# Optimization experiments

Measured on AMD Instinct MI355X. Metric: run time of the kernel, lower is better.

## Reference

```python
import jax, jax.numpy as jnp
import numpy as np

B, S, D = 128, 512, 512  # source requires S == hidden_dim for bmm(Q^T, K^T) to type-check


def setup_inputs() -> dict:
    key = jax.random.key(0)
    ks = jax.random.split(key, 7)
    scale = 1.0 / np.sqrt(D)
    return {
        "x": jax.random.normal(ks[0], (B, S, D), dtype=jnp.float32),
        "Wq": jax.random.uniform(ks[1], (D, D), jnp.float32, -scale, scale),
        "bq": jax.random.uniform(ks[2], (D,), jnp.float32, -scale, scale),
        "Wk": jax.random.uniform(ks[3], (D, D), jnp.float32, -scale, scale),
        "bk": jax.random.uniform(ks[4], (D,), jnp.float32, -scale, scale),
        "Wv": jax.random.uniform(ks[5], (D, D), jnp.float32, -scale, scale),
        "bv": jax.random.uniform(ks[6], (D,), jnp.float32, -scale, scale),
    }


def reference(x, Wq, bq, Wk, bk, Wv, bv):
    # nn.Linear: y = x @ W^T + b
    Q = jnp.einsum("bsd,ed->bse", x, Wq) + bq  # (B,S,D)
    K = jnp.einsum("bsd,ed->bse", x, Wk) + bk
    V = jnp.einsum("bsd,ed->bse", x, Wv) + bv
    Qp = jnp.transpose(Q, (0, 2, 1))  # (B,D,S)
    Kp = jnp.transpose(K, (0, 2, 1))  # (B,D,S); bmm needs S == D
    energy = jnp.matmul(Qp, Kp)       # (B,D,D) -- unscaled, as in source
    attention = jax.nn.softmax(energy, axis=2)
    Vp = jnp.transpose(V, (0, 2, 1))  # (B,D,S)
    context = jnp.matmul(attention, Vp)  # (B,D,S)
    return jnp.transpose(context, (0, 2, 1))  # (B,S,D)
```

## Files before the change

kernel.cpp:

```cpp
#include <hip/hip_runtime.h>
#include <hip/hip_bf16.h>


#define NDIM 512
#define NBATCH 128
constexpr size_t SD = (size_t)NDIM * NDIM;

typedef __attribute__((ext_vector_type(8))) short bf16x8;
typedef __attribute__((ext_vector_type(4))) float f32x4;

typedef const __attribute__((address_space(1))) unsigned int* gas_ptr;
typedef __attribute__((address_space(3))) unsigned int* las_ptr;

struct alignas(8) us4 { unsigned short x, y, z, w; };

__device__ __forceinline__ void gl_lds16(const void* g, void* lds) {
    __builtin_amdgcn_global_load_lds((gas_ptr)g, (las_ptr)lds, 16, 0, 0);
}
__device__ __forceinline__ unsigned short f2bf(float x) {
    return __builtin_bit_cast(unsigned short, __float2bfloat16(x));
}
__device__ __forceinline__ float bf2f(unsigned short u) {
    return __bfloat162float(__builtin_bit_cast(__hip_bfloat16, u));
}

template<int EPI, int BIAS>
__global__ __launch_bounds__(512, 2) void gemm8_fused3(
    const unsigned short* aH, const unsigned short* aL, long sA,
    const unsigned short* bH, const unsigned short* bL, long sB,
    void* c0v, void* c1v, long sC, const float* __restrict__ bias)
{
    constexpr int NTK = 16;
    __shared__ unsigned short AHs[2][8192];
    __shared__ unsigned short ALs[2][8192];
    __shared__ unsigned short BHs[2][8192];
    __shared__ unsigned short BLs[2][8192];

    const int nwg = gridDim.x;
    int id = blockIdx.x;
    int wg = ((nwg & 7) == 0) ? ((id & 7) * (nwg >> 3) + (id >> 3)) : id;
    const int z  = wg >> 2;
    const int m0 = ((wg >> 1) & 1) * 256;
    const int n0 = (wg & 1) * 256;

    const int tid = threadIdx.x;
    const int l = tid & 63, w = tid >> 6;
    const int wr = w >> 2, wc = w & 3;

    const unsigned short* gAH = aH + (size_t)z * sA + (size_t)m0 * NDIM;
    const unsigned short* gAL = aL + (size_t)z * sA + (size_t)m0 * NDIM;
    const unsigned short* gBH = bH + (size_t)z * sB + (size_t)n0 * NDIM;
    const unsigned short* gBL = bL + (size_t)z * sB + (size_t)n0 * NDIM;

    auto stage = [&](const unsigned short* g, unsigned short* panel, int kt) {
        const int k0 = kt << 5;
        #pragma unroll
        for (int s = 0; s < 2; ++s) {
            const int G = s * 512 + tid;
            const int r = G >> 2, gp = G & 3;
            gl_lds16(g + (size_t)r * NDIM + k0 + ((gp ^ ((r >> 1) & 3)) << 3),
                     panel + G * 8);
        }
    };
    auto readA = [&](const unsigned short* panel, bf16x8 (&dst)[2][4]) {
        #pragma unroll
        for (int H = 0; H < 2; ++H)
            #pragma unroll
            for (int mi = 0; mi < 4; ++mi) {
                const int row = H * 128 + wr * 64 + mi * 16 + (l & 15);
                const int gp = (l >> 4) ^ ((row >> 1) & 3);
                dst[H][mi] = *(const bf16x8*)&panel[row * 32 + gp * 8];
            }
    };
    auto readB = [&](const unsigned short* panel, bf16x8 (&dst)[2][2]) {
        #pragma unroll
        for (int H = 0; H < 2; ++H)
            #pragma unroll
            for (int ni = 0; ni < 2; ++ni) {
                const int row = H * 128 + wc * 32 + ni * 16 + (l & 15);
                const int gp = (l >> 4) ^ ((row >> 1) & 3);
                dst[H][ni] = *(const bf16x8*)&panel[row * 32 + gp * 8];
            }
    };

    f32x4 acc[2][2][4][2] = {};

    auto mfma32 = [&](const bf16x8 (&a)[2][4], const bf16x8 (&b)[2][2]) {
        __builtin_amdgcn_s_setprio(1);
        #pragma unroll
        for (int Qr = 0; Qr < 2; ++Qr)
            #pragma unroll
            for (int Qc = 0; Qc < 2; ++Qc)
                #pragma unroll
                for (int mi = 0; mi < 4; ++mi)
                    #pragma unroll
                    for (int ni = 0; ni < 2; ++ni)
                        acc[Qr][Qc][mi][ni] = __builtin_amdgcn_mfma_f32_16x16x32_bf16(
                            a[Qr][mi], b[Qc][ni], acc[Qr][Qc][mi][ni], 0, 0, 0);
        __builtin_amdgcn_s_setprio(0);
    };

    stage(gAH, AHs[0], 0); stage(gBH, BHs[0], 0);
    stage(gAL, ALs[0], 0); stage(gBL, BLs[0], 0);
    asm volatile("s_waitcnt vmcnt(4)" ::: "memory");
    asm volatile("s_barrier" ::: "memory");

    for (int kt = 0; kt < NTK; ++kt) {
        const int cur = kt & 1, nxt = cur ^ 1;
        const int ktn = (kt + 1 < NTK) ? kt + 1 : kt;
        bf16x8 ah[2][4], al[2][4], bh[2][2], bl[2][2];

        readA(AHs[cur], ah); readB(BHs[cur], bh);
        stage(gAH, AHs[nxt], ktn); stage(gBH, BHs[nxt], ktn);
        asm volatile("s_waitcnt vmcnt(6)" ::: "memory");
        asm volatile("s_barrier" ::: "memory");
        asm volatile("s_waitcnt lgkmcnt(0)" ::: "memory");
        __builtin_amdgcn_sched_barrier(0);
        mfma32(ah, bh);

        readA(ALs[cur], al);
        stage(gAL, ALs[nxt], ktn);
        asm volatile("s_waitcnt vmcnt(6)" ::: "memory");
        asm volatile("s_barrier" ::: "memory");
        asm volatile("s_waitcnt lgkmcnt(0)" ::: "memory");
        __builtin_amdgcn_sched_barrier(0);
        mfma32(al, bh);

        readB(BLs[cur], bl);
        stage(gBL, BLs[nxt], ktn);
        asm volatile("s_waitcnt vmcnt(4)" ::: "memory");
        asm volatile("s_barrier" ::: "memory");
        asm volatile("s_waitcnt lgkmcnt(0)" ::: "memory");
        __builtin_amdgcn_sched_barrier(0);
        mfma32(ah, bl);
    }
    asm volatile("s_waitcnt vmcnt(0) lgkmcnt(0)" ::: "memory");

    const size_t zc = (size_t)z * sC;
    const int cr = (l >> 4) << 2;
    const int cc = l & 15;

    if constexpr (EPI == 3) {
        float* red  = (float*)&AHs[0][0];
        float* red2 = red + 1024;
        float2* stats = (float2*)c1v;
        const int h = n0 >> 8;
        __syncthreads();
        #pragma unroll
        for (int Qr = 0; Qr < 2; ++Qr)
            #pragma unroll
            for (int mi = 0; mi < 4; ++mi)
                #pragma unroll
                for (int r = 0; r < 4; ++r) {
                    float v = fmaxf(fmaxf(acc[Qr][0][mi][0][r], acc[Qr][0][mi][1][r]),
                                    fmaxf(acc[Qr][1][mi][0][r], acc[Qr][1][mi][1][r]));
                    #pragma unroll
                    for (int s = 1; s < 16; s <<= 1) v = fmaxf(v, __shfl_xor(v, s, 64));
                    const int row = Qr * 128 + wr * 64 + mi * 16 + cr + r;
                    if ((l & 15) == 0) red[row * 4 + wc] = v;
                }
        __syncthreads();
        #pragma unroll
        for (int Qr = 0; Qr < 2; ++Qr)
            #pragma unroll
            for (int mi = 0; mi < 4; ++mi)
                #pragma unroll
                for (int r = 0; r < 4; ++r) {
                    const int row = Qr * 128 + wr * 64 + mi * 16 + cr + r;
                    const float mb = fmaxf(fmaxf(red[row * 4], red[row * 4 + 1]),
                                           fmaxf(red[row * 4 + 2], red[row * 4 + 3]));
                    float sum = 0.0f;
                    #pragma unroll
                    for (int Qc = 0; Qc < 2; ++Qc)
                        #pragma unroll
                        for (int ni = 0; ni < 2; ++ni) {
                            const float e = __expf(acc[Qr][Qc][mi][ni][r] - mb);
                            acc[Qr][Qc][mi][ni][r] = e;
                            sum += e;
                        }
                    #pragma unroll
                    for (int s = 1; s < 16; s <<= 1) sum += __shfl_xor(sum, s, 64);
                    if ((l & 15) == 0) red2[row * 4 + wc] = sum;
                }
        __syncthreads();
        #pragma unroll
        for (int Qr = 0; Qr < 2; ++Qr)
            #pragma unroll
            for (int mi = 0; mi < 4; ++mi)
                #pragma unroll
                for (int r = 0; r < 4; ++r) {
                    const int row = Qr * 128 + wr * 64 + mi * 16 + cr + r;
                    if (wc == 0 && (l & 15) == 0) {
                        const float mb = fmaxf(fmaxf(red[row * 4], red[row * 4 + 1]),
                                               fmaxf(red[row * 4 + 2], red[row * 4 + 3]));
                        const float sb = red2[row * 4] + red2[row * 4 + 1]
                                       + red2[row * 4 + 2] + red2[row * 4 + 3];
                        stats[((size_t)z * NDIM + m0 + row) * 2 + h] = make_float2(mb, sb);
                    }
                    const int m = m0 + row;
                    #pragma unroll
                    for (int Qc = 0; Qc < 2; ++Qc)
                        #pragma unroll
                        for (int ni = 0; ni < 2; ++ni) {
                            const int n = n0 + Qc * 128 + wc * 32 + ni * 16 + cc;
                            ((unsigned short*)c0v)[zc + (size_t)m * NDIM + n] =
                                f2bf(acc[Qr][Qc][mi][ni][r]);
                        }
                }
        return;
    }

    #pragma unroll
    for (int Qr = 0; Qr < 2; ++Qr) {
        #pragma unroll
        for (int Qc = 0; Qc < 2; ++Qc) {
            #pragma unroll
            for (int mi = 0; mi < 4; ++mi) {
                #pragma unroll
                for (int r = 0; r < 4; ++r) {
                    const int m = m0 + Qr * 128 + wr * 64 + mi * 16 + cr + r;
                    const float bm = (BIAS == 1) ? bias[m] : 0.0f;
                    #pragma unroll
                    for (int ni = 0; ni < 2; ++ni) {
                        const int n = n0 + Qc * 128 + wc * 32 + ni * 16 + cc;
                        float v = acc[Qr][Qc][mi][ni][r] + bm + ((BIAS == 2) ? bias[n] : 0.0f);
                        const size_t idx = zc + (size_t)m * NDIM + n;
                        if (EPI == 0) {
                            ((float*)c0v)[idx] = v;
                        } else if (EPI == 1) {
                            ((unsigned short*)c0v)[idx] = f2bf(v);
                        } else {
                            const unsigned short hh = f2bf(v);
                            ((unsigned short*)c0v)[idx] = hh;
                            ((unsigned short*)c1v)[idx] = f2bf(v - bf2f(hh));
                        }
                    }
                }
            }
        }
    }
}

template<int NSEG, int EPI, int BIAS>
__global__ __launch_bounds__(512, 2) void gemm8_nt(
    const unsigned short* a0, const unsigned short* a1, const unsigned short* a2, long sA,
    const unsigned short* b0, const unsigned short* b1, const unsigned short* b2, long sB,
    void* c0v, void* c1v, long sC, const float* __restrict__ bias)
{
    constexpr int NTK = NSEG * 8;
    __shared__ unsigned short AS[2][256 * 64];
    __shared__ unsigned short BS[2][256 * 64];

    const int nwg = gridDim.x;
    int id = blockIdx.x;
    int wg = ((nwg & 7) == 0) ? ((id & 7) * (nwg >> 3) + (id >> 3)) : id;
    const int z  = wg >> 2;
    const int m0 = ((wg >> 1) & 1) * 256;
    const int n0 = (wg & 1) * 256;

    const int tid = threadIdx.x;
    const int l = tid & 63, w = tid >> 6;
    const int wr = w >> 2, wc = w & 3;

    const size_t zA = (size_t)z * sA + (size_t)m0 * NDIM;
    const size_t zB = (size_t)z * sB + (size_t)n0 * NDIM;

    const int srow = tid >> 3;
    const int scol = (((tid & 7) ^ ((tid >> 3) & 7)) << 3);
    const int ldst = tid * 8;

    auto segA = [&](int s) {
        const unsigned short* p = a0;
        if constexpr (NSEG > 1) { if (s == 1) p = a1; }
        if constexpr (NSEG > 2) { if (s == 2) p = a2; }
        return p;
    };
    auto segB = [&](int s) {
        const unsigned short* p = b0;
        if constexpr (NSEG > 1) { if (s == 1) p = b1; }
        if constexpr (NSEG > 2) { if (s == 2) p = b2; }
        return p;
    };
    auto stageA = [&](int kt, int H, int slot) {
        const int seg = kt >> 3, k0 = (kt & 7) << 6;
        const unsigned short* g = segA(seg) + zA;
        #pragma unroll
        for (int j = 0; j < 2; ++j)
            gl_lds16(g + (size_t)(H * 128 + j * 64 + srow) * NDIM + k0 + scol,
                     &AS[slot][H * 8192 + j * 4096 + ldst]);
    };
    auto stageB = [&](int kt, int H, int slot) {
        const int seg = kt >> 3, k0 = (kt & 7) << 6;
        const unsigned short* g = segB(seg) + zB;
        #pragma unroll
        for (int j = 0; j < 2; ++j)
            gl_lds16(g + (size_t)(H * 128 + j * 64 + srow) * NDIM + k0 + scol,
                     &BS[slot][H * 8192 + j * 4096 + ldst]);
    };

    auto readA = [&](int slot, int H, bf16x8 (&dst)[4][2]) {
        #pragma unroll
        for (int mi = 0; mi < 4; ++mi) {
            const int row = H * 128 + wr * 64 + mi * 16 + (l & 15);
            #pragma unroll
            for (int kk = 0; kk < 2; ++kk) {
                const int s16 = ((kk << 2) + (l >> 4)) ^ (l & 7);
                dst[mi][kk] = *(const bf16x8*)&AS[slot][row * 64 + s16 * 8];
            }
        }
    };
    auto readB = [&](int slot, int H, bf16x8 (&dst)[2][2]) {
        #pragma unroll
        for (int ni = 0; ni < 2; ++ni) {
            const int row = H * 128 + wc * 32 + ni * 16 + (l & 15);
            #pragma unroll
            for (int kk = 0; kk < 2; ++kk) {
                const int s16 = ((kk << 2) + (l >> 4)) ^ (l & 7);
                dst[ni][kk] = *(const bf16x8*)&BS[slot][row * 64 + s16 * 8];
            }
        }
    };
    auto mfma16 = [&](f32x4 (&ac)[4][2], const bf16x8 (&a)[4][2],
                      const bf16x8 (&b)[2][2]) {
        __builtin_amdgcn_s_setprio(1);
        #pragma unroll
        for (int mi = 0; mi < 4; ++mi)
            #pragma unroll
            for (int ni = 0; ni < 2; ++ni)
                #pragma unroll
                for (int kk = 0; kk < 2; ++kk)
                    ac[mi][ni] = __builtin_amdgcn_mfma_f32_16x16x32_bf16(
                        a[mi][kk], b[ni][kk], ac[mi][ni], 0, 0, 0);
        __builtin_amdgcn_s_setprio(0);
    };

    f32x4 acc[2][2][4][2] = {};

    stageA(0, 0, 0); stageB(0, 0, 0); stageB(0, 1, 0); stageA(0, 1, 0);
    asm volatile("s_waitcnt vmcnt(4)" ::: "memory");
    asm volatile("s_barrier" ::: "memory");

    for (int kt = 0; kt < NTK; ++kt) {
        const int cur = kt & 1, nxt = cur ^ 1;
        const int ktn = (kt + 1 < NTK) ? kt + 1 : kt;
        bf16x8 a0f[4][2], a1f[4][2], b0f[2][2], b1f[2][2];

        readA(cur, 0, a0f); readB(cur, 0, b0f);
        stageA(ktn, 0, nxt); stageB(ktn, 0, nxt);
        asm volatile("s_waitcnt vmcnt(6)" ::: "memory");
        asm volatile("s_barrier" ::: "memory");
        asm volatile("s_waitcnt lgkmcnt(0)" ::: "memory");
        __builtin_amdgcn_sched_barrier(0);
        mfma16(acc[0][0], a0f, b0f);

        readB(cur, 1, b1f);
        stageB(ktn, 1, nxt);
        asm volatile("s_waitcnt vmcnt(6)" ::: "memory");
        asm volatile("s_barrier" ::: "memory");
        asm volatile("s_waitcnt lgkmcnt(0)" ::: "memory");
        __builtin_amdgcn_sched_barrier(0);
        mfma16(acc[0][1], a0f, b1f);

        readA(cur, 1, a1f);
        stageA(ktn, 1, nxt);
        asm volatile("s_waitcnt vmcnt(4)" ::: "memory");
        asm volatile("s_barrier" ::: "memory");
        asm volatile("s_waitcnt lgkmcnt(0)" ::: "memory");
        __builtin_amdgcn_sched_barrier(0);
        mfma16(acc[1][1], a1f, b1f);
        mfma16(acc[1][0], a1f, b0f);
    }
    asm volatile("s_waitcnt vmcnt(0) lgkmcnt(0)" ::: "memory");

    const size_t zc = (size_t)z * sC;
    const int cr = (l >> 4) << 2;
    const int cc = l & 15;
    #pragma unroll
    for (int Qr = 0; Qr < 2; ++Qr) {
        #pragma unroll
        for (int Qc = 0; Qc < 2; ++Qc) {
            #pragma unroll
            for (int mi = 0; mi < 4; ++mi) {
                #pragma unroll
                for (int r = 0; r < 4; ++r) {
                    const int m = m0 + Qr * 128 + wr * 64 + mi * 16 + cr + r;
                    const float bm = (BIAS == 1) ? bias[m] : 0.0f;
                    #pragma unroll
                    for (int ni = 0; ni < 2; ++ni) {
                        const int n = n0 + Qc * 128 + wc * 32 + ni * 16 + cc;
                        float v = acc[Qr][Qc][mi][ni][r] + bm + ((BIAS == 2) ? bias[n] : 0.0f);
                        const size_t idx = zc + (size_t)m * NDIM + n;
                        if (EPI == 0) {
                            ((float*)c0v)[idx] = v;
                        } else if (EPI == 1) {
                            ((unsigned short*)c0v)[idx] = f2bf(v);
                        } else {
                            const unsigned short hh = f2bf(v);
                            ((unsigned short*)c0v)[idx] = hh;
                            ((unsigned short*)c1v)[idx] = f2bf(v - bf2f(hh));
                        }
                    }
                }
            }
        }
    }
}

template<int NSEG, int EPI, int BIAS>
__global__ __launch_bounds__(256) void gemm_bf16_nt(
    const unsigned short* a0, const unsigned short* a1, const unsigned short* a2, long sA,
    const unsigned short* b0, const unsigned short* b1, const unsigned short* b2, long sB,
    void* c0v, void* c1v, long sC, const float* __restrict__ bias)
{
    __shared__ unsigned short As[128 * 64];
    __shared__ unsigned short Bs[128 * 64];

    const int z  = blockIdx.z;
    const int m0 = blockIdx.y * 128, n0 = blockIdx.x * 128;
    const int tid = threadIdx.x;
    const int l = tid & 63, w = tid >> 6;
    const int wr = w >> 1, wc = w & 1;

    const int srow = tid >> 3;
    const int scol = (tid & 7) << 3;
    unsigned short* ldsA = &As[tid * 8];
    unsigned short* ldsB = &Bs[tid * 8];

    f32x4 acc[4][4] = {};

    const unsigned short* Asegs[3] = {a0, a1, a2};
    const unsigned short* Bsegs[3] = {b0, b1, b2};

    #pragma unroll
    for (int s = 0; s < NSEG; ++s) {
        const unsigned short* Ab = Asegs[s] + (size_t)z * sA + (size_t)m0 * NDIM;
        const unsigned short* Bb = Bsegs[s] + (size_t)z * sB + (size_t)n0 * NDIM;
        for (int k0 = 0; k0 < NDIM; k0 += 64) {
            __syncthreads();
            #pragma unroll
            for (int i = 0; i < 4; ++i) {
                gl_lds16(Ab + (size_t)(srow + i * 32) * NDIM + k0 + scol, ldsA + i * 2048);
                gl_lds16(Bb + (size_t)(srow + i * 32) * NDIM + k0 + scol, ldsB + i * 2048);
            }
            __syncthreads();
            #pragma unroll
            for (int kk = 0; kk < 2; ++kk) {
                bf16x8 af[4], bfv[4];
                #pragma unroll
                for (int f = 0; f < 4; ++f) {
                    af[f]  = *(const bf16x8*)&As[(wr * 64 + f * 16 + (l & 15)) * 64 + kk * 32 + (l >> 4) * 8];
                    bfv[f] = *(const bf16x8*)&Bs[(wc * 64 + f * 16 + (l & 15)) * 64 + kk * 32 + (l >> 4) * 8];
                }
                #pragma unroll
                for (int mi = 0; mi < 4; ++mi)
                    #pragma unroll
                    for (int ni = 0; ni < 4; ++ni)
                        acc[mi][ni] = __builtin_amdgcn_mfma_f32_16x16x32_bf16(
                            af[mi], bfv[ni], acc[mi][ni], 0, 0, 0);
            }
        }
    }

    const size_t zc = (size_t)z * sC;
    const int cr = (l >> 4) << 2;
    const int cc = l & 15;
    #pragma unroll
    for (int mi = 0; mi < 4; ++mi) {
        #pragma unroll
        for (int r = 0; r < 4; ++r) {
            const int m = m0 + wr * 64 + mi * 16 + cr + r;
            const float bm = (BIAS == 1) ? bias[m] : 0.0f;
            #pragma unroll
            for (int ni = 0; ni < 4; ++ni) {
                const int n = n0 + wc * 64 + ni * 16 + cc;
                float v = acc[mi][ni][r] + bm + ((BIAS == 2) ? bias[n] : 0.0f);
                const size_t idx = zc + (size_t)m * NDIM + n;
                if (EPI == 0) {
                    ((float*)c0v)[idx] = v;
                } else if (EPI == 1) {
                    ((unsigned short*)c0v)[idx] = f2bf(v);
                } else {
                    const unsigned short hh = f2bf(v);
                    ((unsigned short*)c0v)[idx] = hh;
                    ((unsigned short*)c1v)[idx] = f2bf(v - bf2f(hh));
                }
            }
        }
    }
}

__global__ __launch_bounds__(256) void scaleP(
    unsigned short* __restrict__ P, const float2* __restrict__ stats)
{
    const int l  = threadIdx.x & 63;
    const int wv = threadIdx.x >> 6;
    const size_t row = (size_t)blockIdx.x * 4 + wv;
    unsigned short* p = P + row * NDIM;

    const float2 st0 = stats[row * 2];
    const float2 st1 = stats[row * 2 + 1];
    const float M = fmaxf(st0.x, st1.x);
    const float S = st0.y * __expf(st0.x - M) + st1.y * __expf(st1.x - M);
    const float f = __expf(((l < 32) ? st0.x : st1.x) - M) / S;

    us4 a = ((us4*)p)[l * 2], b = ((us4*)p)[l * 2 + 1];
    a.x = f2bf(bf2f(a.x) * f); a.y = f2bf(bf2f(a.y) * f);
    a.z = f2bf(bf2f(a.z) * f); a.w = f2bf(bf2f(a.w) * f);
    b.x = f2bf(bf2f(b.x) * f); b.y = f2bf(bf2f(b.y) * f);
    b.z = f2bf(bf2f(b.z) * f); b.w = f2bf(bf2f(b.w) * f);
    ((us4*)p)[l * 2]     = a;
    ((us4*)p)[l * 2 + 1] = b;
}

__global__ __launch_bounds__(256) void softmax_bf16(
    const float* __restrict__ E, unsigned short* __restrict__ A)
{
    const int l  = threadIdx.x & 63;
    const int wv = threadIdx.x >> 6;
    const size_t row = (size_t)blockIdx.x * 4 + wv;
    const float* p = E + row * NDIM;
    unsigned short* q = A + row * NDIM;

    const float4 v0 = ((const float4*)p)[l * 2];
    const float4 v1 = ((const float4*)p)[l * 2 + 1];

    float mx = fmaxf(fmaxf(fmaxf(v0.x, v0.y), fmaxf(v0.z, v0.w)),
                     fmaxf(fmaxf(v1.x, v1.y), fmaxf(v1.z, v1.w)));
    #pragma unroll
    for (int s = 32; s > 0; s >>= 1) mx = fmaxf(mx, __shfl_xor(mx, s, 64));

    float e0 = __expf(v0.x - mx), e1 = __expf(v0.y - mx);
    float e2 = __expf(v0.z - mx), e3 = __expf(v0.w - mx);
    float e4 = __expf(v1.x - mx), e5 = __expf(v1.y - mx);
    float e6 = __expf(v1.z - mx), e7 = __expf(v1.w - mx);
    float sm = ((e0 + e1) + (e2 + e3)) + ((e4 + e5) + (e6 + e7));
    #pragma unroll
    for (int s = 32; s > 0; s >>= 1) sm += __shfl_xor(sm, s, 64);

    const float inv = 1.0f / sm;
    us4 o0, o1;
    o0.x = f2bf(e0 * inv); o0.y = f2bf(e1 * inv);
    o0.z = f2bf(e2 * inv); o0.w = f2bf(e3 * inv);
    o1.x = f2bf(e4 * inv); o1.y = f2bf(e5 * inv);
    o1.z = f2bf(e6 * inv); o1.w = f2bf(e7 * inv);
    ((us4*)q)[l * 2]     = o0;
    ((us4*)q)[l * 2 + 1] = o1;
}

template<bool LO>
__global__ __launch_bounds__(256) void split_to_bf16(
    const float* __restrict__ src,
    unsigned short* __restrict__ hi, unsigned short* __restrict__ lo, int n4)
{
    const int i = blockIdx.x * 256 + threadIdx.x;
    if (i >= n4) return;
    const float4 v = ((const float4*)src)[i];
    us4 h;
    h.x = f2bf(v.x); h.y = f2bf(v.y); h.z = f2bf(v.z); h.w = f2bf(v.w);
    ((us4*)hi)[i] = h;
    if (LO) {
        us4 g;
        g.x = f2bf(v.x - bf2f(h.x)); g.y = f2bf(v.y - bf2f(h.y));
        g.z = f2bf(v.z - bf2f(h.z)); g.w = f2bf(v.w - bf2f(h.w));
        ((us4*)lo)[i] = g;
    }
}

extern "C" void kernel_launch(void* const* d_in, const int* in_sizes, int n_in,
                              void* d_out, int out_size, void* d_ws, size_t ws_size,
                              hipStream_t stream)
{
    const float* x  = (const float*)d_in[0];
    const float* Wq = (const float*)d_in[1];
    const float* bq = (const float*)d_in[2];
    const float* Wk = (const float*)d_in[3];
    const float* bk = (const float*)d_in[4];
    const float* Wv = (const float*)d_in[5];
    const float* bv = (const float*)d_in[6];
    float* out = (float*)d_out;

    long units = (long)(ws_size / (2 * SD));
    long cl = (units - 7) / 10;
    if (cl < 1) cl = 1;
    int c = 1;
    while (c * 2 <= cl && c < 128) c *= 2;
    const bool use8 = (c >= 64);
    if (!use8 && c > 32) c = 32;

    unsigned short* p = (unsigned short*)d_ws;
    auto take = [&](size_t elems) { unsigned short* r = p; p += elems; return r; };
    unsigned short* WqH = take(SD);
    unsigned short* WqL = take(SD);
    unsigned short* WkH = take(SD);
    unsigned short* WkL = take(SD);
    unsigned short* WvH = take(SD);
    unsigned short* xH  = take((size_t)c * SD);
    unsigned short* xL  = take((size_t)c * SD);
    unsigned short* QH  = take((size_t)c * SD);
    unsigned short* QL  = take((size_t)c * SD);
    unsigned short* KH  = take((size_t)c * SD);
    unsigned short* KL  = take((size_t)c * SD);
    unsigned short* Vb  = take((size_t)c * SD);
    unsigned short* Ab  = take((size_t)c * SD);
    unsigned short* stats_u = take((size_t)c * 4096);
    float2* stats = (float2*)stats_u;
    float* Ew = (float*)p;

    const int n4w = (int)(SD / 4);
    split_to_bf16<true ><<<dim3((n4w + 255) / 256), dim3(256), 0, stream>>>(Wq, WqH, WqL, n4w);
    split_to_bf16<true ><<<dim3((n4w + 255) / 256), dim3(256), 0, stream>>>(Wk, WkH, WkL, n4w);
    split_to_bf16<false><<<dim3((n4w + 255) / 256), dim3(256), 0, stream>>>(Wv, WvH, nullptr, n4w);

    for (int b0 = 0; b0 < NBATCH; b0 += c) {
        const int cb = (NBATCH - b0 < c) ? (NBATCH - b0) : c;
        const int n4 = (int)((size_t)cb * SD / 4);
        split_to_bf16<true><<<dim3((n4 + 255) / 256), dim3(256), 0, stream>>>(
            x + (size_t)b0 * SD, xH, xL, n4);

        if (use8) {
            const dim3 g(4 * cb), blk(512);
            gemm8_fused3<2, 1><<<g, blk, 0, stream>>>(
                WqH, WqL, 0,  xH, xL, (long)SD,  QH, QL, (long)SD, bq);
            gemm8_fused3<2, 2><<<g, blk, 0, stream>>>(
                xH, xL, (long)SD,  WkH, WkL, 0,  KH, KL, (long)SD, bk);
            gemm8_nt<1, 1, 2><<<g, blk, 0, stream>>>(
                xH, nullptr, nullptr, (long)SD,  WvH, nullptr, nullptr, 0,  Vb, nullptr, (long)SD, bv);
            gemm8_fused3<3, 0><<<g, blk, 0, stream>>>(
                QH, QL, (long)SD,  KH, KL, (long)SD,  Ab, stats, (long)SD, nullptr);
            scaleP<<<dim3(cb * NDIM / 4), dim3(256), 0, stream>>>(Ab, stats);
            gemm8_nt<1, 0, 0><<<g, blk, 0, stream>>>(
                Vb, nullptr, nullptr, (long)SD,  Ab, nullptr, nullptr, (long)SD,
                out + (size_t)b0 * SD, nullptr, (long)SD, nullptr);
        } else {
            const dim3 g(4, 4, cb), blk(256);
            gemm_bf16_nt<3, 2, 1><<<g, blk, 0, stream>>>(
                WqH, WqL, WqH, 0,  xH, xH, xL, (long)SD,  QH, QL, (long)SD, bq);
            gemm_bf16_nt<3, 2, 2><<<g, blk, 0, stream>>>(
                xH, xL, xH, (long)SD,  WkH, WkH, WkL, 0,  KH, KL, (long)SD, bk);
            gemm_bf16_nt<1, 1, 2><<<g, blk, 0, stream>>>(
                xH, nullptr, nullptr, (long)SD,  WvH, nullptr, nullptr, 0,  Vb, nullptr, (long)SD, bv);
            gemm_bf16_nt<3, 0, 0><<<g, blk, 0, stream>>>(
                QH, QL, QH, (long)SD,  KH, KH, KL, (long)SD,  Ew, nullptr, (long)SD, nullptr);
            softmax_bf16<<<dim3(cb * NDIM / 4), dim3(256), 0, stream>>>(Ew, Ab);
            gemm_bf16_nt<1, 0, 0><<<g, blk, 0, stream>>>(
                Vb, nullptr, nullptr, (long)SD,  Ab, nullptr, nullptr, (long)SD,
                out + (size_t)b0 * SD, nullptr, (long)SD, nullptr);
        }
    }
}
```

Before: 529.6 us.

## Fold softmax normalization into PV GEMM via per-half rescale factors

Removes the scaleP pass, which read and rewrote the whole bf16 probability matrix to apply the softmax normalization. A tiny prep_fac kernel now turns the per-row-half max/sum stats into two factors. The PV GEMM rescales its accumulators at the half-K boundary (kt==4) and multiplies by the final normalizer in the epilogue. This saves a full read and write of P per batch chunk, at the cost of an extra small kernel and a register-wide rescale inside the GEMM loop; bf16 rounding now happens on unnormalized probabilities.

```diff
diff --git a/kernel.cpp b/kernel.cpp
--- a/kernel.cpp
+++ b/kernel.cpp
@@ -210,6 +210,169 @@
         return;
     }
 
+    #pragma unroll
+    for (int Qr = 0; Qr < 2; ++Qr) {
+        #pragma unroll
+        for (int Qc = 0; Qc < 2; ++Qc) {
+            #pragma unroll
+            for (int mi = 0; mi < 4; ++mi) {
+                #pragma unroll
+                for (int r = 0; r < 4; ++r) {
+                    const int m = m0 + Qr * 128 + wr * 64 + mi * 16 + cr + r;
+                    const float bm = (BIAS == 1) ? bias[m] : 0.0f;
+                    #pragma unroll
+                    for (int ni = 0; ni < 2; ++ni) {
+                        const int n = n0 + Qc * 128 + wc * 32 + ni * 16 + cc;
+                        float v = acc[Qr][Qc][mi][ni][r] + bm + ((BIAS == 2) ? bias[n] : 0.0f);
+                        const size_t idx = zc + (size_t)m * NDIM + n;
+                        if (EPI == 1) {
+                            ((unsigned short*)c0v)[idx] = f2bf(v);
+                        } else {
+                            const unsigned short hh = f2bf(v);
+                            ((unsigned short*)c0v)[idx] = hh;
+                            ((unsigned short*)c1v)[idx] = f2bf(v - bf2f(hh));
+                        }
+                    }
+                }
+            }
+        }
+    }
+}
+
+template<int NSEG, int EPI, int BIAS>
+__global__ __launch_bounds__(512, 2) void gemm8_nt(
+    const unsigned short* a0, const unsigned short* a1, const unsigned short* a2, long sA,
+    const unsigned short* b0, const unsigned short* b1, const unsigned short* b2, long sB,
+    void* c0v, void* c1v, long sC, const float* __restrict__ bias)
+{
+    constexpr int NTK = NSEG * 8;
+    __shared__ unsigned short AS[2][256 * 64];
+    __shared__ unsigned short BS[2][256 * 64];
+
+    const int nwg = gridDim.x;
+    int id = blockIdx.x;
+    int wg = ((nwg & 7) == 0) ? ((id & 7) * (nwg >> 3) + (id >> 3)) : id;
+    const int z  = wg >> 2;
+    const int m0 = ((wg >> 1) & 1) * 256;
+    const int n0 = (wg & 1) * 256;
+
+    const int tid = threadIdx.x;
+    const int l = tid & 63, w = tid >> 6;
+    const int wr = w >> 2, wc = w & 3;
+
+    const size_t zA = (size_t)z * sA + (size_t)m0 * NDIM;
+    const size_t zB = (size_t)z * sB + (size_t)n0 * NDIM;
+
+    const int srow = tid >> 3;
+    const int scol = (((tid & 7) ^ ((tid >> 3) & 7)) << 3);
+    const int ldst = tid * 8;
+
+    auto segA = [&](int s) {
+        const unsigned short* p = a0;
+        if constexpr (NSEG > 1) { if (s == 1) p = a1; }
+        if constexpr (NSEG > 2) { if (s == 2) p = a2; }
+        return p;
+    };
+    auto segB = [&](int s) {
+        const unsigned short* p = b0;
+        if constexpr (NSEG > 1) { if (s == 1) p = b1; }
+        if constexpr (NSEG > 2) { if (s == 2) p = b2; }
+        return p;
+    };
+    auto stageA = [&](int kt, int H, int slot) {
+        const int seg = kt >> 3, k0 = (kt & 7) << 6;
+        const unsigned short* g = segA(seg) + zA;
+        #pragma unroll
+        for (int j = 0; j < 2; ++j)
+            gl_lds16(g + (size_t)(H * 128 + j * 64 + srow) * NDIM + k0 + scol,
+                     &AS[slot][H * 8192 + j * 4096 + ldst]);
+    };
+    auto stageB = [&](int kt, int H, int slot) {
+        const int seg = kt >> 3, k0 = (kt & 7) << 6;
+        const unsigned short* g = segB(seg) + zB;
+        #pragma unroll
+        for (int j = 0; j < 2; ++j)
+            gl_lds16(g + (size_t)(H * 128 + j * 64 + srow) * NDIM + k0 + scol,
+                     &BS[slot][H * 8192 + j * 4096 + ldst]);
+    };
+
+    auto readA = [&](int slot, int H, bf16x8 (&dst)[4][2]) {
+        #pragma unroll
+        for (int mi = 0; mi < 4; ++mi) {
+            const int row = H * 128 + wr * 64 + mi * 16 + (l & 15);
+            #pragma unroll
+            for (int kk = 0; kk < 2; ++kk) {
+                const int s16 = ((kk << 2) + (l >> 4)) ^ (l & 7);
+                dst[mi][kk] = *(const bf16x8*)&AS[slot][row * 64 + s16 * 8];
+            }
+        }
+    };
+    auto readB = [&](int slot, int H, bf16x8 (&dst)[2][2]) {
+        #pragma unroll
+        for (int ni = 0; ni < 2; ++ni) {
+            const int row = H * 128 + wc * 32 + ni * 16 + (l & 15);
+            #pragma unroll
+            for (int kk = 0; kk < 2; ++kk) {
+                const int s16 = ((kk << 2) + (l >> 4)) ^ (l & 7);
+                dst[ni][kk] = *(const bf16x8*)&BS[slot][row * 64 + s16 * 8];
+            }
+        }
+    };
+    auto mfma16 = [&](f32x4 (&ac)[4][2], const bf16x8 (&a)[4][2],
+                      const bf16x8 (&b)[2][2]) {
+        __builtin_amdgcn_s_setprio(1);
+        #pragma unroll
+        for (int mi = 0; mi < 4; ++mi)
+            #pragma unroll
+            for (int ni = 0; ni < 2; ++ni)
+                #pragma unroll
+                for (int kk = 0; kk < 2; ++kk)
+                    ac[mi][ni] = __builtin_amdgcn_mfma_f32_16x16x32_bf16(
+                        a[mi][kk], b[ni][kk], ac[mi][ni], 0, 0, 0);
+        __builtin_amdgcn_s_setprio(0);
+    };
+
+    f32x4 acc[2][2][4][2] = {};
+
+    stageA(0, 0, 0); stageB(0, 0, 0); stageB(0, 1, 0); stageA(0, 1, 0);
+    asm volatile("s_waitcnt vmcnt(4)" ::: "memory");
+    asm volatile("s_barrier" ::: "memory");
+
+    for (int kt = 0; kt < NTK; ++kt) {
+        const int cur = kt & 1, nxt = cur ^ 1;
+        const int ktn = (kt + 1 < NTK) ? kt + 1 : kt;
+        bf16x8 a0f[4][2], a1f[4][2], b0f[2][2], b1f[2][2];
+
+        readA(cur, 0, a0f); readB(cur, 0, b0f);
+        stageA(ktn, 0, nxt); stageB(ktn, 0, nxt);
+        asm volatile("s_waitcnt vmcnt(6)" ::: "memory");
+        asm volatile("s_barrier" ::: "memory");
+        asm volatile("s_waitcnt lgkmcnt(0)" ::: "memory");
+        __builtin_amdgcn_sched_barrier(0);
+        mfma16(acc[0][0], a0f, b0f);
+
+        readB(cur, 1, b1f);
+        stageB(ktn, 1, nxt);
+        asm volatile("s_waitcnt vmcnt(6)" ::: "memory");
+        asm volatile("s_barrier" ::: "memory");
+        asm volatile("s_waitcnt lgkmcnt(0)" ::: "memory");
+        __builtin_amdgcn_sched_barrier(0);
+        mfma16(acc[0][1], a0f, b1f);
+
+        readA(cur, 1, a1f);
+        stageA(ktn, 1, nxt);
+        asm volatile("s_waitcnt vmcnt(4)" ::: "memory");
+        asm volatile("s_barrier" ::: "memory");
+        asm volatile("s_waitcnt lgkmcnt(0)" ::: "memory");
+        __builtin_amdgcn_sched_barrier(0);
+        mfma16(acc[1][1], a1f, b1f);
+        mfma16(acc[1][0], a1f, b0f);
+    }
+    asm volatile("s_waitcnt vmcnt(0) lgkmcnt(0)" ::: "memory");
+
+    const size_t zc = (size_t)z * sC;
+    const int cr = (l >> 4) << 2;
+    const int cc = l & 15;
     #pragma unroll
     for (int Qr = 0; Qr < 2; ++Qr) {
         #pragma unroll
@@ -241,13 +404,12 @@
     }
 }
 
-template<int NSEG, int EPI, int BIAS>
-__global__ __launch_bounds__(512, 2) void gemm8_nt(
-    const unsigned short* a0, const unsigned short* a1, const unsigned short* a2, long sA,
-    const unsigned short* b0, const unsigned short* b1, const unsigned short* b2, long sB,
-    void* c0v, void* c1v, long sC, const float* __restrict__ bias)
+__global__ __launch_bounds__(512, 2) void gemm8_pv(
+    const unsigned short* a0, long sA,
+    const unsigned short* b0, long sB,
+    float* c0, long sC, const float2* __restrict__ fac)
 {
-    constexpr int NTK = NSEG * 8;
+    constexpr int NTK = 8;
     __shared__ unsigned short AS[2][256 * 64];
     __shared__ unsigned short BS[2][256 * 64];
 
@@ -261,6 +423,14 @@
     const int tid = threadIdx.x;
     const int l = tid & 63, w = tid >> 6;
     const int wr = w >> 2, wc = w & 3;
+    const int cc = l & 15;
+
+    float2 facv[2][2];
+    #pragma unroll
+    for (int Qc = 0; Qc < 2; ++Qc)
+        #pragma unroll
+        for (int ni = 0; ni < 2; ++ni)
+            facv[Qc][ni] = fac[(size_t)z * NDIM + n0 + Qc * 128 + wc * 32 + ni * 16 + cc];
 
     const size_t zA = (size_t)z * sA + (size_t)m0 * NDIM;
     const size_t zB = (size_t)z * sB + (size_t)n0 * NDIM;
@@ -269,35 +439,20 @@
     const int scol = (((tid & 7) ^ ((tid >> 3) & 7)) << 3);
     const int ldst = tid * 8;
 
-    auto segA = [&](int s) {
-        const unsigned short* p = a0;
-        if constexpr (NSEG > 1) { if (s == 1) p = a1; }
-        if constexpr (NSEG > 2) { if (s == 2) p = a2; }
-        return p;
-    };
-    auto segB = [&](int s) {
-        const unsigned short* p = b0;
-        if constexpr (NSEG > 1) { if (s == 1) p = b1; }
-        if constexpr (NSEG > 2) { if (s == 2) p = b2; }
-        return p;
-    };
     auto stageA = [&](int kt, int H, int slot) {
-        const int seg = kt >> 3, k0 = (kt & 7) << 6;
-        const unsigned short* g = segA(seg) + zA;
+        const int k0 = kt << 6;
         #pragma unroll
         for (int j = 0; j < 2; ++j)
-            gl_lds16(g + (size_t)(H * 128 + j * 64 + srow) * NDIM + k0 + scol,
+            gl_lds16(a0 + zA + (size_t)(H * 128 + j * 64 + srow) * NDIM + k0 + scol,
                      &AS[slot][H * 8192 + j * 4096 + ldst]);
     };
     auto stageB = [&](int kt, int H, int slot) {
-        const int seg = kt >> 3, k0 = (kt & 7) << 6;
-        const unsigned short* g = segB(seg) + zB;
+        const int k0 = kt << 6;
         #pragma unroll
         for (int j = 0; j < 2; ++j)
-            gl_lds16(g + (size_t)(H * 128 + j * 64 + srow) * NDIM + k0 + scol,
+            gl_lds16(b0 + zB + (size_t)(H * 128 + j * 64 + srow) * NDIM + k0 + scol,
                      &BS[slot][H * 8192 + j * 4096 + ldst]);
     };
-
     auto readA = [&](int slot, int H, bf16x8 (&dst)[4][2]) {
         #pragma unroll
         for (int mi = 0; mi < 4; ++mi) {
@@ -320,6 +475,9 @@
             }
         }
     };
+
+    f32x4 acc[2][2][4][2] = {};
+
     auto mfma16 = [&](f32x4 (&ac)[4][2], const bf16x8 (&a)[4][2],
                       const bf16x8 (&b)[2][2]) {
         __builtin_amdgcn_s_setprio(1);
@@ -334,8 +492,6 @@
         __builtin_amdgcn_s_setprio(0);
     };
 
-    f32x4 acc[2][2][4][2] = {};
-
     stageA(0, 0, 0); stageB(0, 0, 0); stageB(0, 1, 0); stageA(0, 1, 0);
     asm volatile("s_waitcnt vmcnt(4)" ::: "memory");
     asm volatile("s_barrier" ::: "memory");
@@ -345,6 +501,20 @@
         const int ktn = (kt + 1 < NTK) ? kt + 1 : kt;
         bf16x8 a0f[4][2], a1f[4][2], b0f[2][2], b1f[2][2];
 
+        if (kt == 4) {
+            #pragma unroll
+            for (int Qr = 0; Qr < 2; ++Qr)
+                #pragma unroll
+                for (int Qc = 0; Qc < 2; ++Qc)
+                    #pragma unroll
+                    for (int mi = 0; mi < 4; ++mi)
+                        #pragma unroll
+                        for (int ni = 0; ni < 2; ++ni)
+                            #pragma unroll
+                            for (int r = 0; r < 4; ++r)
+                                acc[Qr][Qc][mi][ni][r] *= facv[Qc][ni].x;
+        }
+
         readA(cur, 0, a0f); readB(cur, 0, b0f);
         stageA(ktn, 0, nxt); stageB(ktn, 0, nxt);
         asm volatile("s_waitcnt vmcnt(6)" ::: "memory");
@@ -374,36 +544,33 @@
 
     const size_t zc = (size_t)z * sC;
     const int cr = (l >> 4) << 2;
-    const int cc = l & 15;
     #pragma unroll
-    for (int Qr = 0; Qr < 2; ++Qr) {
-        #pragma unroll
-        for (int Qc = 0; Qc < 2; ++Qc) {
-            #pragma unroll
-            for (int mi = 0; mi < 4; ++mi) {
+    for (int Qr = 0; Qr < 2; ++Qr)
+        #pragma unroll
+        for (int Qc = 0; Qc < 2; ++Qc)
+            #pragma unroll
+            for (int mi = 0; mi < 4; ++mi)
                 #pragma unroll
                 for (int r = 0; r < 4; ++r) {
                     const int m = m0 + Qr * 128 + wr * 64 + mi * 16 + cr + r;
-                    const float bm = (BIAS == 1) ? bias[m] : 0.0f;
                     #pragma unroll
                     for (int ni = 0; ni < 2; ++ni) {
                         const int n = n0 + Qc * 128 + wc * 32 + ni * 16 + cc;
-                        float v = acc[Qr][Qc][mi][ni][r] + bm + ((BIAS == 2) ? bias[n] : 0.0f);
-                        const size_t idx = zc + (size_t)m * NDIM + n;
-                        if (EPI == 0) {
-                            ((float*)c0v)[idx] = v;
-                        } else if (EPI == 1) {
-                            ((unsigned short*)c0v)[idx] = f2bf(v);
-                        } else {
-                            const unsigned short hh = f2bf(v);
-                            ((unsigned short*)c0v)[idx] = hh;
-                            ((unsigned short*)c1v)[idx] = f2bf(v - bf2f(hh));
-                        }
+                        c0[zc + (size_t)m * NDIM + n] =
+                            acc[Qr][Qc][mi][ni][r] * facv[Qc][ni].y;
                     }
                 }
-            }
-        }
-    }
+}
+
+__global__ __launch_bounds__(256) void prep_fac(
+    const float2* __restrict__ stats, float2* __restrict__ fac, int nrows)
+{
+    const int i = blockIdx.x * 256 + threadIdx.x;
+    if (i >= nrows) return;
+    const float2 s0 = stats[i * 2], s1 = stats[i * 2 + 1];
+    const float M = fmaxf(s0.x, s1.x);
+    const float S = s0.y * __expf(s0.x - M) + s1.y * __expf(s1.x - M);
+    fac[i] = make_float2(__expf(s0.x - s1.x), __expf(s1.x - M) / S);
 }
 
 template<int NSEG, int EPI, int BIAS>
@@ -487,29 +654,6 @@
             }
         }
     }
-}
-
-__global__ __launch_bounds__(256) void scaleP(
-    unsigned short* __restrict__ P, const float2* __restrict__ stats)
-{
-    const int l  = threadIdx.x & 63;
-    const int wv = threadIdx.x >> 6;
-    const size_t row = (size_t)blockIdx.x * 4 + wv;
-    unsigned short* p = P + row * NDIM;
-
-    const float2 st0 = stats[row * 2];
-    const float2 st1 = stats[row * 2 + 1];
-    const float M = fmaxf(st0.x, st1.x);
-    const float S = st0.y * __expf(st0.x - M) + st1.y * __expf(st1.x - M);
-    const float f = __expf(((l < 32) ? st0.x : st1.x) - M) / S;
-
-    us4 a = ((us4*)p)[l * 2], b = ((us4*)p)[l * 2 + 1];
-    a.x = f2bf(bf2f(a.x) * f); a.y = f2bf(bf2f(a.y) * f);
-    a.z = f2bf(bf2f(a.z) * f); a.w = f2bf(bf2f(a.w) * f);
-    b.x = f2bf(bf2f(b.x) * f); b.y = f2bf(bf2f(b.y) * f);
-    b.z = f2bf(bf2f(b.z) * f); b.w = f2bf(bf2f(b.w) * f);
-    ((us4*)p)[l * 2]     = a;
-    ((us4*)p)[l * 2 + 1] = b;
 }
 
 __global__ __launch_bounds__(256) void softmax_bf16(
@@ -580,7 +724,7 @@
     float* out = (float*)d_out;
 
     long units = (long)(ws_size / (2 * SD));
-    long cl = (units - 7) / 10;
+    long cl = (units - 8) / 10;
     if (cl < 1) cl = 1;
     int c = 1;
     while (c * 2 <= cl && c < 128) c *= 2;
@@ -602,8 +746,8 @@
     unsigned short* KL  = take((size_t)c * SD);
     unsigned short* Vb  = take((size_t)c * SD);
     unsigned short* Ab  = take((size_t)c * SD);
-    unsigned short* stats_u = take((size_t)c * 4096);
-    float2* stats = (float2*)stats_u;
+    float2* stats = (float2*)take((size_t)c * 4096);
+    float2* fac   = (float2*)take((size_t)c * 2048);
     float* Ew = (float*)p;
 
     const int n4w = (int)(SD / 4);
@@ -627,10 +771,11 @@
                 xH, nullptr, nullptr, (long)SD,  WvH, nullptr, nullptr, 0,  Vb, nullptr, (long)SD, bv);
             gemm8_fused3<3, 0><<<g, blk, 0, stream>>>(
                 QH, QL, (long)SD,  KH, KL, (long)SD,  Ab, stats, (long)SD, nullptr);
-            scaleP<<<dim3(cb * NDIM / 4), dim3(256), 0, stream>>>(Ab, stats);
-            gemm8_nt<1, 0, 0><<<g, blk, 0, stream>>>(
-                Vb, nullptr, nullptr, (long)SD,  Ab, nullptr, nullptr, (long)SD,
-                out + (size_t)b0 * SD, nullptr, (long)SD, nullptr);
+            prep_fac<<<dim3((cb * NDIM + 255) / 256), dim3(256), 0, stream>>>(
+                stats, fac, cb * NDIM);
+            gemm8_pv<<<g, blk, 0, stream>>>(
+                Vb, (long)SD,  Ab, (long)SD,
+                out + (size_t)b0 * SD, (long)SD, fac);
         } else {
             const dim3 g(4, 4, cb), blk(256);
             gemm_bf16_nt<3, 2, 1><<<g, blk, 0, stream>>>(
```

Result: faster. 508.9 us (-3.9%).
